# Kernel tuning notes

Hardware: AMD Instinct MI355X
Metric: run time of the kernel (lower is better)

Reference implementation:

```python
import jax, jax.numpy as jnp
import numpy as np

B, D, E, NF, FD, H = 8192, 1024, 6, 32, 32, 256
MINK, MAXK = 1, 4

def _lin(a, w, b):
    return a @ w.T + b

def setup_inputs():
    key = jax.random.key(0)
    it = iter(jax.random.split(key, 60))
    def nrm(shape, s=0.02):
        return jax.random.normal(next(it), shape, jnp.float32) * s
    z = lambda *s: jnp.zeros(s, jnp.float32)
    return dict(
        x=jax.random.normal(next(it), (B, D), jnp.float32),
        esp_patterns=nrm((E, D), 1.0),
        sim_w1=nrm((D // 2, D)), sim_b1=z(D // 2),
        sim_w2=nrm((E, D // 2)), sim_b2=z(E),
        rout_w1=nrm((D // 2, D + E)), rout_b1=z(D // 2),
        rout_w2=nrm((E, D // 2)), rout_b2=z(E),
        kpred_w1=nrm((16, 6)), kpred_b1=z(16),
        kpred_w2=nrm((1, 16)), kpred_b2=z(1),
        sp_v_w=nrm((D, D)), sp_v_b=z(D),
        sp_o_w=nrm((D, D)), sp_o_b=z(D),
        sp_q1_w=nrm((D, D)), sp_q1_b=z(D),
        sp_q2_w=nrm((D, D)), sp_q2_b=z(D),
        de_w1=nrm((H, D)), de_b1=z(H),
        de_w2=nrm((D, H)), de_b2=z(D),
        de_g_w=nrm((D, D)), de_g_b=z(D),
        cf_in_w=nrm((3 * FD, FD)), cf_in_b=z(3 * FD),
        cf_o_w=nrm((FD, FD)), cf_o_b=z(FD),
        cf_f_w=nrm((FD, FD)), cf_f_b=z(FD),
        hf_w1=nrm((H, D)), hf_b1=z(H),
        hf_w2=nrm((D, H)), hf_b2=z(D),
        tc_w=nrm((4, 1, 3), 0.2), tc_b=z(4),
        tf_w=nrm((1, 4), 0.2), tf_b=z(1),
        lt_w1=nrm((H, D)), lt_b1=z(H),
        lt_w2=nrm((D, H)), lt_b2=z(D),
        op_w=nrm((D, D)), op_b=z(D),
    )

def reference(x, esp_patterns, sim_w1, sim_b1, sim_w2, sim_b2, rout_w1, rout_b1, rout_w2, rout_b2,
              kpred_w1, kpred_b1, kpred_w2, kpred_b2, sp_v_w, sp_v_b, sp_o_w, sp_o_b,
              sp_q1_w, sp_q1_b, sp_q2_w, sp_q2_b, de_w1, de_b1, de_w2, de_b2, de_g_w, de_g_b,
              cf_in_w, cf_in_b, cf_o_w, cf_o_b, cf_f_w, cf_f_b, hf_w1, hf_b1, hf_w2, hf_b2,
              tc_w, tc_b, tf_w, tf_b, lt_w1, lt_b1, lt_w2, lt_b2, op_w, op_b):
    # ---- FeatureAnalyzer ----
    sparsity = (x == 0).astype(jnp.float32).mean(-1)
    var_u = jnp.var(x, axis=-1, ddof=1)            # torch default unbiased var
    magnitude = jnp.abs(x).max(-1)
    norm = jnp.linalg.norm(x, axis=-1)
    mean = x.mean(-1, keepdims=True)
    std = jnp.sqrt(var_u[:, None] + 1e-8)
    skew = (((x - mean) / std) ** 3).mean(-1)
    s_abs = -jnp.sort(-jnp.abs(x), axis=-1)        # descending
    top20 = int(0.2 * D)
    conc = s_abs[:, :top20].sum(-1) / (s_abs.sum(-1) + 1e-8)
    feats = jnp.stack([sparsity, var_u, magnitude, norm, skew, conc], -1)  # (B,6)
    # ---- IntelligentRouter ----
    spec = jax.nn.sigmoid(x @ esp_patterns.T + _lin(jax.nn.relu(_lin(x, sim_w1, sim_b1)), sim_w2, sim_b2))
    probs = jax.nn.softmax(_lin(jax.nn.relu(_lin(jnp.concatenate([x, spec], -1), rout_w1, rout_b1)), rout_w2, rout_b2), -1)
    k_ratio = jax.nn.sigmoid(_lin(jax.nn.relu(_lin(feats, kpred_w1, kpred_b1)), kpred_w2, kpred_b2))[:, 0]
    k_vals = MINK + (MAXK - MINK) * k_ratio
    k = jnp.clip(jnp.floor(jnp.median(k_vals)), MINK, MAXK).astype(jnp.int32)  # int(median) truncation
    tp, ti = jax.lax.top_k(probs, MAXK)
    gmask = jnp.arange(MAXK) < k
    gates = jax.nn.softmax(jnp.where(gmask, tp, -jnp.inf), -1)  # (B,MAXK)
    # ---- experts (eval mode: dropout = identity) ----
    # SparseQuadraticExpert: seq-len-1 MHA collapses to V->out projections
    att = _lin(_lin(x, sp_v_w, sp_v_b), sp_o_w, sp_o_b)
    e_sp = _lin(jax.nn.relu(_lin(att * x, sp_q1_w, sp_q1_b)), sp_q2_w, sp_q2_b)
    # DenseQuadraticExpert
    e_de = _lin(jax.nn.relu(_lin(x, de_w1, de_b1)), de_w2, de_b2) + jax.nn.sigmoid(_lin(x, de_g_w, de_g_b)) * x
    # CrossFieldQuadraticExpert: single-head attention over fields
    xf = x.reshape(-1, NF, FD)
    q, kk, v = jnp.split(_lin(xf, cf_in_w, cf_in_b), 3, axis=-1)
    attn = jax.nn.softmax(jnp.einsum('bqd,bkd->bqk', q, kk) / jnp.sqrt(jnp.float32(FD)), -1)
    att_f = _lin(jnp.einsum('bqk,bkd->bqd', attn, v), cf_o_w, cf_o_b)
    e_cf = _lin(att_f * xf, cf_f_w, cf_f_b).reshape(-1, D)
    # HighFreqQuadraticExpert
    filt = _lin(jnp.tanh(_lin(x, hf_w1, hf_b1)), hf_w2, hf_b2)
    e_hf = x + (filt - x) * x
    # TemporalQuadraticExpert (AdaptiveAvgPool1d(D) on length-D input == identity)
    conv = jax.nn.relu(jax.lax.conv_general_dilated(x[:, None, :], tc_w, (1,), [(1, 1)], dimension_numbers=('NCH', 'OIH', 'NCH')) + tc_b[None, :, None])
    wts = jax.nn.sigmoid(_lin(conv.transpose(0, 2, 1), tf_w, tf_b))[..., 0]  # (B,D)
    e_tp = (x * wts) * x
    # LongTailQuadraticExpert
    t = _lin(jax.nn.elu(_lin(x, lt_w1, lt_b1)), lt_w2, lt_b2)
    e_lt = jnp.sign(x) * jnp.sqrt(jnp.abs(t * x) + 1e-8)
    # ---- dispatch + combine ----
    stack = jnp.stack([e_sp, e_de, e_cf, e_hf, e_tp, e_lt], axis=1)  # (B,E,D)
    sel = jnp.take_along_axis(stack, ti[:, :, None], axis=1)         # (B,MAXK,D)
    comb = (gates[:, :, None] * sel).sum(1)
    return _lin(comb, op_w, op_b) + x  # output projection + residual; Identity norm (batch_norm=False)
```

## Files before the change

kernel.cpp:

```cpp
#include <hip/hip_runtime.h>
#include <stdint.h>

typedef unsigned short u16;
typedef __attribute__((ext_vector_type(2))) float f32x2;
typedef __attribute__((ext_vector_type(4))) float f32x4;
typedef __attribute__((ext_vector_type(4))) unsigned short u16x4;
typedef __attribute__((ext_vector_type(8))) short short8;

#define DEV static __device__ __forceinline__

DEV float bf2f(u16 u){ union{unsigned int i; float f;} v; v.i=((unsigned int)u)<<16; return v.f; }
DEV u16 f2bf(float f){ union{float f; unsigned int i;} v; v.f=f; unsigned int u=v.i;
  return (u16)((u + 0x7FFFu + ((u>>16)&1u))>>16); }
DEV float wred(float v){ for(int o=32;o;o>>=1) v += __shfl_xor(v,o); return v; }
DEV float wredmax(float v){ for(int o=32;o;o>>=1) v = fmaxf(v,__shfl_xor(v,o)); return v; }
DEV int wredi(int v){ for(int o=32;o;o>>=1) v += __shfl_xor(v,o); return v; }

DEV void gload16(const void* g, void* l){
  __builtin_amdgcn_global_load_lds((const __attribute__((address_space(1))) unsigned int*)g,
                                   (__attribute__((address_space(3))) unsigned int*)l, 16, 0, 0);
}

DEV float actf(int ACT, float v){
  if(ACT==1) return v>0.f?v:0.f;
  if(ACT==2) return 1.f/(1.f+__expf(-v));
  if(ACT==3) return tanhf(v);
  if(ACT==4) return v>0.f?v:(__expf(v)-1.f);
  return v;
}

__global__ void cvt_kernel(const float* __restrict__ s, u16* __restrict__ d, int n4){
  for(int i=blockIdx.x*blockDim.x+threadIdx.x; i<n4; i+=gridDim.x*blockDim.x){
    f32x4 v=((const f32x4*)s)[i];
    u16x4 o;
    #pragma unroll
    for(int j=0;j<4;++j) o[j]=f2bf(v[j]);
    ((u16x4*)d)[i]=o;
  }
}

__global__ void cvt6_kernel(
    const float* __restrict__ s0, const float* __restrict__ s1, const float* __restrict__ s2,
    const float* __restrict__ s3, const float* __restrict__ s4, const float* __restrict__ s5,
    u16* __restrict__ d0, u16* __restrict__ d1, u16* __restrict__ d2,
    u16* __restrict__ d3, u16* __restrict__ d4, u16* __restrict__ d5, int n4each){
  const float* ss[6]={s0,s1,s2,s3,s4,s5};
  u16* dd[6]={d0,d1,d2,d3,d4,d5};
  const int total=6*n4each;
  for(int i=blockIdx.x*blockDim.x+threadIdx.x; i<total; i+=gridDim.x*blockDim.x){
    int b=i/n4each, r=i-b*n4each;
    f32x4 v=((const f32x4*)ss[b])[r];
    u16x4 o;
    #pragma unroll
    for(int j=0;j<4;++j) o[j]=f2bf(v[j]);
    ((u16x4*)dd[b])[r]=o;
  }
}

__global__ void cvt_split(const float* __restrict__ s, u16* __restrict__ hi, u16* __restrict__ lo, int n4){
  for(int i=blockIdx.x*blockDim.x+threadIdx.x; i<n4; i+=gridDim.x*blockDim.x){
    f32x4 v=((const f32x4*)s)[i];
    u16x4 h,l;
    #pragma unroll
    for(int j=0;j<4;++j){ h[j]=f2bf(v[j]); l[j]=f2bf(v[j]-bf2f(h[j])); }
    ((u16x4*)hi)[i]=h; ((u16x4*)lo)[i]=l;
  }
}

__global__ void cvt_split_rw1(const float* __restrict__ src, u16* __restrict__ hi, u16* __restrict__ lo){
  for(int i=blockIdx.x*blockDim.x+threadIdx.x; i<512*1024; i+=gridDim.x*blockDim.x){
    int r=i>>10, c=i&1023;
    float v=src[(size_t)r*1030+c];
    u16 h=f2bf(v);
    hi[i]=h; lo[i]=f2bf(v-bf2f(h));
  }
}

__global__ __launch_bounds__(256) void transpose_bf(const float* __restrict__ src, u16* __restrict__ dst){
  __shared__ float t[32][33];
  const int bx=blockIdx.x&31, by=blockIdx.x>>5;
  const int lx=threadIdx.x&31, ly=threadIdx.x>>5;
  #pragma unroll
  for(int r=0;r<4;++r)
    t[ly+8*r][lx] = src[(size_t)(by*32+ly+8*r)*1024 + bx*32+lx];
  __syncthreads();
  #pragma unroll
  for(int r=0;r<4;++r)
    dst[(size_t)(bx*32+ly+8*r)*1024 + by*32+lx] = f2bf(t[lx][ly+8*r]);
}

__global__ __launch_bounds__(256) void bias_comp(const float* __restrict__ ow, const float* __restrict__ vb,
    const float* __restrict__ ob, float* __restrict__ bc){
  const int wv=threadIdx.x>>6, lane=threadIdx.x&63;
  const int rowi=blockIdx.x*4+wv;
  float s=0.f;
  const float* wr=ow+(size_t)rowi*1024;
  #pragma unroll
  for(int j=0;j<16;++j) s+=wr[j*64+lane]*vb[j*64+lane];
  s=wred(s);
  if(lane==0) bc[rowi]=ob[rowi]+s;
}

__global__ void pack_b768(const float* __restrict__ b0, const float* __restrict__ b1,
                          const float* __restrict__ b2, float* __restrict__ o){
  int i=blockIdx.x*blockDim.x+threadIdx.x;
  if(i<256) o[i]=b0[i];
  else if(i<512) o[i]=b1[i-256];
  else if(i<768) o[i]=b2[i-512];
}

__global__ void pack_b1024(const float* __restrict__ b0, const float* __restrict__ b1, float* __restrict__ o){
  int i=blockIdx.x*blockDim.x+threadIdx.x;
  if(i<512) o[i]=b0[i];
  else if(i<1024) o[i]=b1[i-512];
}

template<int ACT, int EPI>
__global__ __launch_bounds__(256) void gemm_bt(
    const u16* __restrict__ A, const u16* __restrict__ W,
    const float* __restrict__ bias, const u16* __restrict__ auxb,
    const float* __restrict__ auxf, const float* __restrict__ wsel,
    u16* __restrict__ comb, void* __restrict__ Cv, int M, int N, int K, int lda)
{
  __shared__ __align__(16) u16 lA[128*64];
  __shared__ __align__(16) u16 lB[128*64];
  const int tid=threadIdx.x, lane=tid&63, wv=tid>>6;
  const int wr=wv>>1, wc=wv&1;
  const int gx=gridDim.x;
  const int nwg=gx*gridDim.y;
  const int flat=blockIdx.y*gx+blockIdx.x;
  const int chunk=nwg>>3;
  const int nf=(flat&7)*chunk + (flat>>3);
  const int bn=(nf%gx)*128, bm=(nf/gx)*128;
  f32x4 acc[4][4];
  #pragma unroll
  for(int m=0;m<4;++m){
    #pragma unroll
    for(int n=0;n<4;++n) acc[m][n]=(f32x4)0.f;
  }
  const int srow = wv*8 + (lane>>3);
  const int scol = (lane&7)*8;
  for(int kt=0;kt<K;kt+=64){
    #pragma unroll
    for(int i=0;i<4;++i){
      gload16(A + (size_t)(bm + i*32 + srow)*lda + kt + scol, &lA[(i*32 + wv*8)*64]);
      gload16(W + (size_t)(bn + i*32 + srow)*K + kt + scol, &lB[(i*32 + wv*8)*64]);
    }
    __syncthreads();
    #pragma unroll
    for(int kk=0;kk<2;++kk){
      const int fr=lane&15, kc=kk*32+(lane>>4)*8;
      short8 af[4], bfr[4];
      #pragma unroll
      for(int m=0;m<4;++m) af[m]=*(const short8*)&lA[(wr*64+m*16+fr)*64+kc];
      #pragma unroll
      for(int n=0;n<4;++n) bfr[n]=*(const short8*)&lB[(wc*64+n*16+fr)*64+kc];
      #pragma unroll
      for(int m=0;m<4;++m){
        #pragma unroll
        for(int n=0;n<4;++n)
          acc[m][n]=__builtin_amdgcn_mfma_f32_16x16x32_bf16(af[m],bfr[n],acc[m][n],0,0,0);
      }
    }
    __syncthreads();
  }
  const int fr=lane&15, fq=lane>>4;
  #pragma unroll
  for(int m=0;m<4;++m){
    #pragma unroll
    for(int n=0;n<4;++n){
      const int col = bn + wc*64 + n*16 + fr;
      const float bv = bias ? bias[col] : 0.f;
      #pragma unroll
      for(int j=0;j<4;++j){
        const int row = bm + wr*64 + m*16 + fq*4 + j;
        const size_t idx = (size_t)row*N+col;
        float v = acc[m][n][j] + bv;
        if(ACT==5){
          v = (col<256) ? fmaxf(v,0.f) : (col<512 ? tanhf(v) : (v>0.f?v:(__expf(v)-1.f)));
        } else v = actf(ACT, v);
        if(EPI==0){ ((u16*)Cv)[idx]=f2bf(v); }
        else if(EPI==1){ ((float*)Cv)[idx]=v; }
        else if(EPI==2){ ((u16*)Cv)[idx]=f2bf(v*bf2f(auxb[idx])); }
        else if(EPI==3){ comb[idx]=f2bf(wsel[row*6+0]*v); }
        else if(EPI==4){ comb[idx]=f2bf(bf2f(comb[idx])+wsel[row*6+1]*(v + bf2f(auxb[idx])*auxf[idx])); }
        else if(EPI==5){ float x0=bf2f(auxb[idx]); comb[idx]=f2bf(bf2f(comb[idx])+wsel[row*6+3]*(x0+(v-x0)*x0)); }
        else if(EPI==6){
          float x0=bf2f(auxb[idx]);
          float sg=(x0>0.f)?1.f:((x0<0.f)?-1.f:0.f);
          comb[idx]=f2bf(bf2f(comb[idx])+wsel[row*6+5]*sg*sqrtf(fabsf(v*x0)+1e-8f));
        }
        else { ((float*)Cv)[idx]=v+auxf[idx]; }
      }
    }
  }
}

__global__ __launch_bounds__(256) void gemm_split2(
    const u16* __restrict__ Ah, const u16* __restrict__ Al,
    const u16* __restrict__ Wh, const u16* __restrict__ Wl,
    const float* __restrict__ bias, float* __restrict__ C, int M, int N, int K)
{
  const int LDL=40;
  __shared__ __align__(16) u16 lAh[128*40], lAl[128*40], lBh[128*40], lBl[128*40];
  const int tid=threadIdx.x, lane=tid&63, wv=tid>>6;
  const int wr=wv>>1, wc=wv&1;
  const int nwg=gridDim.x;
  const int wg=(blockIdx.x%8)*(nwg/8)+blockIdx.x/8;
  const int bx=wg&7, by=wg>>3;
  const int bn=bx*128, bm=by*128;
  f32x4 acc[4][4];
  #pragma unroll
  for(int m=0;m<4;++m){
    #pragma unroll
    for(int n=0;n<4;++n) acc[m][n]=(f32x4)0.f;
  }
  const int srow=tid>>2, scol=(tid&3)*8;
  for(int kt=0;kt<K;kt+=32){
    short8 rah[2],ral[2],rbh[2],rbl[2];
    #pragma unroll
    for(int i=0;i<2;++i){
      size_t ao=(size_t)(bm+i*64+srow)*K+kt+scol;
      size_t bo=(size_t)(bn+i*64+srow)*K+kt+scol;
      rah[i]=*(const short8*)(Ah+ao); ral[i]=*(const short8*)(Al+ao);
      rbh[i]=*(const short8*)(Wh+bo); rbl[i]=*(const short8*)(Wl+bo);
    }
    __syncthreads();
    #pragma unroll
    for(int i=0;i<2;++i){
      int d=(i*64+srow)*LDL+scol;
      *(short8*)&lAh[d]=rah[i]; *(short8*)&lAl[d]=ral[i];
      *(short8*)&lBh[d]=rbh[i]; *(short8*)&lBl[d]=rbl[i];
    }
    __syncthreads();
    const int fr=lane&15, kc=(lane>>4)*8;
    short8 ah[4],al[4],bh[4],bl[4];
    #pragma unroll
    for(int m=0;m<4;++m){ int r=(wr*64+m*16+fr)*LDL+kc; ah[m]=*(const short8*)&lAh[r]; al[m]=*(const short8*)&lAl[r]; }
    #pragma unroll
    for(int n=0;n<4;++n){ int r=(wc*64+n*16+fr)*LDL+kc; bh[n]=*(const short8*)&lBh[r]; bl[n]=*(const short8*)&lBl[r]; }
    #pragma unroll
    for(int m=0;m<4;++m){
      #pragma unroll
      for(int n=0;n<4;++n){
        acc[m][n]=__builtin_amdgcn_mfma_f32_16x16x32_bf16(ah[m],bh[n],acc[m][n],0,0,0);
        acc[m][n]=__builtin_amdgcn_mfma_f32_16x16x32_bf16(ah[m],bl[n],acc[m][n],0,0,0);
        acc[m][n]=__builtin_amdgcn_mfma_f32_16x16x32_bf16(al[m],bh[n],acc[m][n],0,0,0);
      }
    }
  }
  const int fr=lane&15, fq=lane>>4;
  #pragma unroll
  for(int m=0;m<4;++m){
    #pragma unroll
    for(int n=0;n<4;++n){
      const int col = bn + wc*64 + n*16 + fr;
      const float bv = bias[col];
      #pragma unroll
      for(int j=0;j<4;++j){
        const int row = bm + wr*64 + m*16 + fq*4 + j;
        float v = acc[m][n][j] + bv;
        if(col<512) v=fmaxf(v,0.f);
        C[(size_t)row*N+col] = v;
      }
    }
  }
}

__global__ __launch_bounds__(256) void feats_kernel(const float* __restrict__ x,
    const float* __restrict__ kw1, const float* __restrict__ kb1,
    const float* __restrict__ kw2, const float* __restrict__ kb2,
    float* __restrict__ kvals)
{
  const int lane=threadIdx.x&63, wv=threadIdx.x>>6;
  const int row=blockIdx.x*4+wv;
  const float* xr=x+(size_t)row*1024;
  float xv[16]; unsigned int cd[16];
  float s=0.f, ss=0.f, sa=0.f, nz=0.f, amax=0.f;
  #pragma unroll
  for(int t=0;t<4;++t){
    f32x4 v=((const f32x4*)xr)[t*64+lane];
    #pragma unroll
    for(int j=0;j<4;++j){
      float f=v[j];
      union{float f;unsigned int i;} c; c.f=f;
      xv[t*4+j]=f; cd[t*4+j]=c.i&0x7fffffffu;
      s+=f; ss+=f*f; float a=fabsf(f); sa+=a; amax=fmaxf(amax,a); if(f==0.f) nz+=1.f;
    }
  }
  s=wred(s); ss=wred(ss); sa=wred(sa); nz=wred(nz); amax=wredmax(amax);
  const float mean=s/1024.f;
  const float var=(ss - s*mean)/1023.f;
  const float inv=1.f/sqrtf(var+1e-8f);
  float sk=0.f;
  #pragma unroll
  for(int j=0;j<16;++j){ float z=(xv[j]-mean)*inv; sk+=z*z*z; }
  sk=wred(sk);
  unsigned int lo=0u, hi=0x7f800000u;
  while(hi-lo>1u){
    unsigned int mid=(lo+hi)>>1;
    int c=0;
    #pragma unroll
    for(int j=0;j<16;++j) c += (cd[j] >= mid);
    c=wredi(c);
    if(c>=204) lo=mid; else hi=mid;
  }
  const unsigned int T=lo;
  float sg=0.f, cg=0.f;
  #pragma unroll
  for(int j=0;j<16;++j){ if(cd[j] > T){ sg+=fabsf(xv[j]); cg+=1.f; } }
  sg=wred(sg); cg=wred(cg);
  if(lane==0){
    union{unsigned int i;float f;} tv; tv.i=T;
    float conc=(sg + (204.f-cg)*tv.f)/(sa + 1e-8f);
    float feats[6]={ nz/1024.f, var, amax, sqrtf(ss), sk/1024.f, conc };
    float out=kb2[0];
    #pragma unroll
    for(int i=0;i<16;++i){
      float hv=kb1[i];
      #pragma unroll
      for(int j=0;j<6;++j) hv+=kw1[i*6+j]*feats[j];
      hv=fmaxf(hv,0.f);
      out+=kw2[i]*hv;
    }
    kvals[row]=1.f + 3.f*(1.f/(1.f+__expf(-out)));
  }
}

__global__ __launch_bounds__(256) void median_kernel(const float* __restrict__ kvals, int* __restrict__ kint){
  __shared__ unsigned int v[8192];
  __shared__ int hist4[4*257];
  __shared__ unsigned int selT;
  __shared__ int selR;
  const int tid=threadIdx.x, lane=tid&63, wv=tid>>6;
  for(int i=tid;i<8192;i+=256){ union{float f;unsigned int u;} c; c.f=kvals[i]; v[i]=c.u; }
  __syncthreads();
  unsigned int res[2];
  for(int t=0;t<2;++t){
    int r = 8192 - (4096+t) + 1;
    unsigned int prefix=0u;
    for(int lvl=0;lvl<4;++lvl){
      const int shift=24-lvl*8;
      const unsigned int pmask = (lvl==0)?0u:(0xFFFFFFFFu<<(shift+8));
      for(int i=tid;i<4*257;i+=256) hist4[i]=0;
      __syncthreads();
      for(int i=tid;i<8192;i+=256){
        unsigned int c=v[i];
        if((c&pmask)==prefix) atomicAdd(&hist4[wv*257+((c>>shift)&0xFFu)],1);
      }
      __syncthreads();
      if(wv==0){
        int h[4]; int ls=0;
        #pragma unroll
        for(int b=0;b<4;++b){
          int bin=lane*4+b;
          h[b]=hist4[bin]+hist4[257+bin]+hist4[514+bin]+hist4[771+bin];
          ls+=h[b];
        }
        int pfx=ls;
        #pragma unroll
        for(int off=1;off<64;off<<=1){ int tt=__shfl_up(pfx,off); if(lane>=off) pfx+=tt; }
        int total=__shfl(pfx,63);
        int cgt = total - pfx;
        #pragma unroll
        for(int b=3;b>=0;--b){
          if(cgt < r && r <= cgt + h[b]){
            selT = prefix | ((unsigned int)(lane*4+b)<<shift);
            selR = r - cgt;
          }
          cgt += h[b];
        }
      }
      __syncthreads();
      prefix=selT; r=selR;
      __syncthreads();
    }
    res[t]=prefix;
  }
  if(tid==0){
    union{unsigned int u; float f;} a,b; a.u=res[0]; b.u=res[1];
    float med=0.5f*(a.f+b.f);
    int k=(int)floorf(med);
    k = k<1?1:(k>4?4:k);
    *kint=k;
  }
}

__global__ __launch_bounds__(256) void spec_kernel(const float* __restrict__ x, const float* __restrict__ h,
    const float* __restrict__ esp, const float* __restrict__ w2, const float* __restrict__ b2,
    float* __restrict__ spec){
  const int wv=threadIdx.x>>6, lane=threadIdx.x&63;
  const int row=blockIdx.x*4+wv;
  const float* xr=x+(size_t)row*1024;
  const float* hr=h+(size_t)row*1024;
  float xv[16], hv[8];
  #pragma unroll
  for(int j=0;j<16;++j) xv[j]=xr[j*64+lane];
  #pragma unroll
  for(int j=0;j<8;++j) hv[j]=hr[j*64+lane];
  for(int e=0;e<6;++e){
    float s=0.f;
    #pragma unroll
    for(int j=0;j<16;++j) s+=xv[j]*esp[e*1024+j*64+lane];
    #pragma unroll
    for(int j=0;j<8;++j) s+=hv[j]*w2[e*512+j*64+lane];
    s=wred(s);
    if(lane==0) spec[row*6+e]=1.f/(1.f+__expf(-(s+b2[e])));
  }
}

__global__ void rout_fix(float* __restrict__ h, const float* __restrict__ spec, const float* __restrict__ rw1){
  const int total=8192*128;
  for(int i=blockIdx.x*blockDim.x+threadIdx.x;i<total;i+=gridDim.x*blockDim.x){
    int row=i>>7, j0=(i&127)*4;
    const float* sp=&spec[row*6];
    f32x4 hv=*(f32x4*)&h[(size_t)row*1024+512+j0];
    #pragma unroll
    for(int j=0;j<4;++j){
      float v=hv[j];
      int col=j0+j;
      #pragma unroll
      for(int e=0;e<6;++e) v+=sp[e]*rw1[(size_t)col*1030+1024+e];
      hv[j]=fmaxf(v,0.f);
    }
    *(f32x4*)&h[(size_t)row*1024+512+j0]=hv;
  }
}

__global__ __launch_bounds__(256) void probs_kernel(const float* __restrict__ h, const float* __restrict__ w2,
    const float* __restrict__ b2, float* __restrict__ probs){
  const int wv=threadIdx.x>>6, lane=threadIdx.x&63;
  const int row=blockIdx.x*4+wv;
  const float* hr=h+(size_t)row*1024+512;
  float hv[8];
  #pragma unroll
  for(int j=0;j<8;++j) hv[j]=hr[j*64+lane];
  float lg[6];
  #pragma unroll
  for(int e=0;e<6;++e){
    float s=0.f;
    #pragma unroll
    for(int j=0;j<8;++j) s+=hv[j]*w2[e*512+j*64+lane];
    lg[e]=wred(s)+b2[e];
  }
  if(lane==0){
    float m=lg[0];
    #pragma unroll
    for(int e=1;e<6;++e) m=fmaxf(m,lg[e]);
    float den=0.f, ex[6];
    #pragma unroll
    for(int e=0;e<6;++e){ ex[e]=__expf(lg[e]-m); den+=ex[e]; }
    #pragma unroll
    for(int e=0;e<6;++e) probs[row*6+e]=ex[e]/den;
  }
}

__global__ void gates_kernel(const float* __restrict__ probs, const int* __restrict__ kint,
                             float* __restrict__ wsel){
  const int r=blockIdx.x*blockDim.x+threadIdx.x;
  if(r>=8192) return;
  const int k=*kint;
  float p[6];
  #pragma unroll
  for(int e=0;e<6;++e) p[e]=probs[r*6+e];
  float w[6]={0,0,0,0,0,0};
  bool used[6]={false,false,false,false,false,false};
  int idx[4]; float val[4];
  #pragma unroll
  for(int j=0;j<4;++j){
    int bi=0; float bv=-1e30f;
    #pragma unroll
    for(int e=0;e<6;++e) if(!used[e] && p[e]>bv){ bv=p[e]; bi=e; }
    used[bi]=true; idx[j]=bi; val[j]=bv;
  }
  float m=val[0], den=0.f, g[4]={0,0,0,0};
  for(int j=0;j<k;++j){ g[j]=__expf(val[j]-m); den+=g[j]; }
  for(int j=0;j<k;++j) w[idx[j]]=g[j]/den;
  #pragma unroll
  for(int e=0;e<6;++e) wsel[r*6+e]=w[e];
}

__global__ __launch_bounds__(256) void cf_kernel(const float* __restrict__ x,
    const float* __restrict__ w_in, const float* __restrict__ b_in,
    const float* __restrict__ w_o, const float* __restrict__ b_o,
    const float* __restrict__ w_f, const float* __restrict__ b_f,
    const float* __restrict__ wsel, u16* __restrict__ comb){
  __shared__ __align__(16) u16 smem[6400 + 4*6144];
  const int tid=threadIdx.x, wv=tid>>6, lane=tid&63;
  const int fr=lane&15, fq=lane>>4;
  for(int i=tid;i<5120;i+=256){
    float v=(i<3072)? w_in[i] : (i<4096? w_o[i-3072] : w_f[i-4096]);
    smem[(i>>5)*40 + (i&31)] = f2bf(v);
  }
  u16* wb   = smem + 6400 + wv*6144;
  float* xfl= (float*)wb;
  u16* bufA = wb + 2304;
  u16* bufB = bufA + 1280;
  u16* bufC = bufB + 1280;
  const int row = blockIdx.x*4 + wv;
  const float* xr = x + (size_t)row*1024;
  #pragma unroll
  for(int t=0;t<4;++t){
    f32x4 v = ((const f32x4*)xr)[t*64+lane];
    int e=(t*64+lane)*4;
    *(f32x4*)&xfl[(e>>5)*36 + (e&31)] = v;
  }
  __syncthreads();
  short8 xa[2];
  #pragma unroll
  for(int ft=0;ft<2;++ft){
    f32x4 a=*(const f32x4*)&xfl[(ft*16+fr)*36 + fq*8];
    f32x4 b=*(const f32x4*)&xfl[(ft*16+fr)*36 + fq*8 + 4];
    short8 s;
    s[0]=(short)f2bf(a[0]); s[1]=(short)f2bf(a[1]); s[2]=(short)f2bf(a[2]); s[3]=(short)f2bf(a[3]);
    s[4]=(short)f2bf(b[0]); s[5]=(short)f2bf(b[1]); s[6]=(short)f2bf(b[2]); s[7]=(short)f2bf(b[3]);
    xa[ft]=s;
  }
  f32x4 acc1[2][6];
  #pragma unroll
  for(int ct=0;ct<6;++ct){
    short8 wfrag=*(const short8*)&smem[(ct*16+fr)*40 + fq*8];
    #pragma unroll
    for(int ft=0;ft<2;++ft)
      acc1[ft][ct]=__builtin_amdgcn_mfma_f32_16x16x32_bf16(xa[ft],wfrag,(f32x4)0.f,0,0,0);
  }
  float bi[6];
  #pragma unroll
  for(int ct=0;ct<6;++ct) bi[ct]=b_in[ct*16+fr];
  #pragma unroll
  for(int ct=0;ct<6;++ct){
    #pragma unroll
    for(int ft=0;ft<2;++ft){
      #pragma unroll
      for(int j=0;j<4;++j){
        u16 h=f2bf(acc1[ft][ct][j]+bi[ct]);
        int rg=ft*16+fq*4+j, cg=ct*16+fr;
        if(cg<32)      bufA[rg*40+cg]=h;
        else if(cg<64) bufB[rg*40+(cg-32)]=h;
        else           bufC[(cg-64)*40+rg]=h;
      }
    }
  }
  __syncthreads();
  short8 qa0=*(const short8*)&bufA[fr*40+fq*8];
  short8 qa1=*(const short8*)&bufA[(16+fr)*40+fq*8];
  short8 kb0=*(const short8*)&bufB[fr*40+fq*8];
  short8 kb1=*(const short8*)&bufB[(16+fr)*40+fq*8];
  f32x4 aS[2][2];
  aS[0][0]=__builtin_amdgcn_mfma_f32_16x16x32_bf16(qa0,kb0,(f32x4)0.f,0,0,0);
  aS[0][1]=__builtin_amdgcn_mfma_f32_16x16x32_bf16(qa0,kb1,(f32x4)0.f,0,0,0);
  aS[1][0]=__builtin_amdgcn_mfma_f32_16x16x32_bf16(qa1,kb0,(f32x4)0.f,0,0,0);
  aS[1][1]=__builtin_amdgcn_mfma_f32_16x16x32_bf16(qa1,kb1,(f32x4)0.f,0,0,0);
  const float scale=0.17677669529663687f;
  #pragma unroll
  for(int rt=0;rt<2;++rt){
    #pragma unroll
    for(int j=0;j<4;++j){
      float e0=aS[rt][0][j]*scale, e1=aS[rt][1][j]*scale;
      float m=fmaxf(e0,e1);
      #pragma unroll
      for(int o=1;o<16;o<<=1) m=fmaxf(m,__shfl_xor(m,o));
      e0=__expf(e0-m); e1=__expf(e1-m);
      float den=e0+e1;
      #pragma unroll
      for(int o=1;o<16;o<<=1) den+=__shfl_xor(den,o);
      float inv=1.f/den;
      bufA[(rt*16+fq*4+j)*40 + fr]      = f2bf(e0*inv);
      bufA[(rt*16+fq*4+j)*40 + 16+fr]   = f2bf(e1*inv);
    }
  }
  __syncthreads();
  short8 pa0=*(const short8*)&bufA[fr*40+fq*8];
  short8 pa1=*(const short8*)&bufA[(16+fr)*40+fq*8];
  short8 vb0=*(const short8*)&bufC[fr*40+fq*8];
  short8 vb1=*(const short8*)&bufC[(16+fr)*40+fq*8];
  f32x4 aA[2][2];
  aA[0][0]=__builtin_amdgcn_mfma_f32_16x16x32_bf16(pa0,vb0,(f32x4)0.f,0,0,0);
  aA[0][1]=__builtin_amdgcn_mfma_f32_16x16x32_bf16(pa0,vb1,(f32x4)0.f,0,0,0);
  aA[1][0]=__builtin_amdgcn_mfma_f32_16x16x32_bf16(pa1,vb0,(f32x4)0.f,0,0,0);
  aA[1][1]=__builtin_amdgcn_mfma_f32_16x16x32_bf16(pa1,vb1,(f32x4)0.f,0,0,0);
  #pragma unroll
  for(int rt=0;rt<2;++rt)
    #pragma unroll
    for(int dt=0;dt<2;++dt)
      #pragma unroll
      for(int j=0;j<4;++j)
        bufB[(rt*16+fq*4+j)*40 + dt*16+fr]=f2bf(aA[rt][dt][j]);
  __syncthreads();
  short8 aa0=*(const short8*)&bufB[fr*40+fq*8];
  short8 aa1=*(const short8*)&bufB[(16+fr)*40+fq*8];
  short8 ob0=*(const short8*)&smem[(96+fr)*40+fq*8];
  short8 ob1=*(const short8*)&smem[(112+fr)*40+fq*8];
  f32x4 aF[2][2];
  aF[0][0]=__builtin_amdgcn_mfma_f32_16x16x32_bf16(aa0,ob0,(f32x4)0.f,0,0,0);
  aF[0][1]=__builtin_amdgcn_mfma_f32_16x16x32_bf16(aa0,ob1,(f32x4)0.f,0,0,0);
  aF[1][0]=__builtin_amdgcn_mfma_f32_16x16x32_bf16(aa1,ob0,(f32x4)0.f,0,0,0);
  aF[1][1]=__builtin_amdgcn_mfma_f32_16x16x32_bf16(aa1,ob1,(f32x4)0.f,0,0,0);
  float bo[2]={b_o[fr], b_o[16+fr]};
  #pragma unroll
  for(int rt=0;rt<2;++rt){
    #pragma unroll
    for(int dt=0;dt<2;++dt){
      #pragma unroll
      for(int j=0;j<4;++j){
        int fld=rt*16+fq*4+j, d=dt*16+fr;
        float attf=aF[rt][dt][j]+bo[dt];
        bufC[fld*40+d]=f2bf(attf*xfl[fld*36+d]);
      }
    }
  }
  __syncthreads();
  short8 pr0=*(const short8*)&bufC[fr*40+fq*8];
  short8 pr1=*(const short8*)&bufC[(16+fr)*40+fq*8];
  short8 fb0=*(const short8*)&smem[(128+fr)*40+fq*8];
  short8 fb1=*(const short8*)&smem[(144+fr)*40+fq*8];
  f32x4 aE[2][2];
  aE[0][0]=__builtin_amdgcn_mfma_f32_16x16x32_bf16(pr0,fb0,(f32x4)0.f,0,0,0);
  aE[0][1]=__builtin_amdgcn_mfma_f32_16x16x32_bf16(pr0,fb1,(f32x4)0.f,0,0,0);
  aE[1][0]=__builtin_amdgcn_mfma_f32_16x16x32_bf16(pr1,fb0,(f32x4)0.f,0,0,0);
  aE[1][1]=__builtin_amdgcn_mfma_f32_16x16x32_bf16(pr1,fb1,(f32x4)0.f,0,0,0);
  float bff[2]={b_f[fr], b_f[16+fr]};
  const float w2=wsel[row*6+2];
  u16* cb=&comb[(size_t)row*1024];
  #pragma unroll
  for(int rt=0;rt<2;++rt){
    #pragma unroll
    for(int dt=0;dt<2;++dt){
      #pragma unroll
      for(int j=0;j<4;++j){
        int fld=rt*16+fq*4+j, d=dt*16+fr;
        u16 old=cb[fld*32+d];
        cb[fld*32+d]=f2bf(bf2f(old)+w2*(aE[rt][dt][j]+bff[dt]));
      }
    }
  }
}

__global__ __launch_bounds__(256) void tp_kernel(const float* __restrict__ x,
    const float* __restrict__ wsel, const u16* __restrict__ comb,
    const float* __restrict__ tcw, const float* __restrict__ tcb,
    const float* __restrict__ tfw, const float* __restrict__ tfb,
    u16* __restrict__ obf){
  __shared__ float xs[1026];
  const int row=blockIdx.x, tid=threadIdx.x;
  f32x4 u=((const f32x4*)(x+(size_t)row*1024))[tid];
  #pragma unroll
  for(int j=0;j<4;++j) xs[1+4*tid+j]=u[j];
  if(tid==0){ xs[0]=0.f; xs[1025]=0.f; }
  __syncthreads();
  const float w4=wsel[row*6+4];
  float tc[4][3], tb[4], tf[4];
  #pragma unroll
  for(int o=0;o<4;++o){
    #pragma unroll
    for(int kh=0;kh<3;++kh) tc[o][kh]=tcw[o*3+kh];
    tb[o]=tcb[o]; tf[o]=tfw[o];
  }
  const float tfb0=tfb[0];
  u16x4 cv=((const u16x4*)(comb+(size_t)row*1024))[tid];
  u16x4 ov;
  #pragma unroll
  for(int j=0;j<4;++j){
    const int d=4*tid+j;
    float pre=tfb0;
    #pragma unroll
    for(int o=0;o<4;++o){
      float c=tb[o]+tc[o][0]*xs[d]+tc[o][1]*xs[d+1]+tc[o][2]*xs[d+2];
      pre+=tf[o]*fmaxf(c,0.f);
    }
    float wt=1.f/(1.f+__expf(-pre));
    float xv=xs[1+d];
    ov[j]=f2bf(bf2f(cv[j])+w4*xv*xv*wt);
  }
  ((u16x4*)(obf+(size_t)row*1024))[tid]=ov;
}

extern "C" void kernel_launch(void* const* d_in, const int* in_sizes, int n_in,
                              void* d_out, int out_size, void* d_ws, size_t ws_size,
                              hipStream_t stream)
{
  const float* x     =(const float*)d_in[0];
  const float* esp   =(const float*)d_in[1];
  const float* sim_w1=(const float*)d_in[2],  *sim_b1=(const float*)d_in[3];
  const float* sim_w2=(const float*)d_in[4],  *sim_b2=(const float*)d_in[5];
  const float* rout_w1=(const float*)d_in[6], *rout_b1=(const float*)d_in[7];
  const float* rout_w2=(const float*)d_in[8], *rout_b2=(const float*)d_in[9];
  const float* kw1=(const float*)d_in[10], *kb1=(const float*)d_in[11];
  const float* kw2=(const float*)d_in[12], *kb2=(const float*)d_in[13];
  const float* spv_w=(const float*)d_in[14], *spv_b=(const float*)d_in[15];
  const float* spo_w=(const float*)d_in[16], *spo_b=(const float*)d_in[17];
  const float* spq1_w=(const float*)d_in[18], *spq1_b=(const float*)d_in[19];
  const float* spq2_w=(const float*)d_in[20], *spq2_b=(const float*)d_in[21];
  const float* de_w1=(const float*)d_in[22], *de_b1=(const float*)d_in[23];
  const float* de_w2=(const float*)d_in[24], *de_b2=(const float*)d_in[25];
  const float* de_gw=(const float*)d_in[26], *de_gb=(const float*)d_in[27];
  const float* cf_inw=(const float*)d_in[28], *cf_inb=(const float*)d_in[29];
  const float* cf_ow=(const float*)d_in[30], *cf_ob=(const float*)d_in[31];
  const float* cf_fw=(const float*)d_in[32], *cf_fb=(const float*)d_in[33];
  const float* hf_w1=(const float*)d_in[34], *hf_b1=(const float*)d_in[35];
  const float* hf_w2=(const float*)d_in[36], *hf_b2=(const float*)d_in[37];
  const float* tc_w=(const float*)d_in[38], *tc_b=(const float*)d_in[39];
  const float* tf_w=(const float*)d_in[40], *tf_b=(const float*)d_in[41];
  const float* lt_w1=(const float*)d_in[42], *lt_b1=(const float*)d_in[43];
  const float* lt_w2=(const float*)d_in[44], *lt_b2=(const float*)d_in[45];
  const float* op_w=(const float*)d_in[46], *op_b=(const float*)d_in[47];
  float* out=(float*)d_out;
  (void)in_sizes; (void)n_in; (void)out_size; (void)ws_size;

  constexpr int NB=8192;
  const size_t BD=(size_t)NB*1024;
  char* base=(char*)d_ws; size_t off=0;
  auto carve=[&](size_t n)->void*{ void* q=base+off; off+=(n+255)&~(size_t)255; return q; };
  u16*  comb =(u16*)carve(BD*2);
  u16*  bufA =(u16*)carve(BD*2);
  u16*  bufB =(u16*)carve(BD*2);
  u16*  x_hi =(u16*)carve(BD*2);
  u16*  x_lo =(u16*)carve(BD*2);
  float* h1024=(float*)carve(BD*4);
  u16*  h768 =(u16*)carve((size_t)NB*768*2);
  u16* w1024h=(u16*)carve((size_t)1024*1024*2);
  u16* w1024l=(u16*)carve((size_t)1024*1024*2);
  u16* spv_bf =(u16*)carve((size_t)1024*1024*2);
  u16* spo_bf =(u16*)carve((size_t)1024*1024*2);
  u16* spq1_bf=(u16*)carve((size_t)1024*1024*2);
  u16* spq2_bf=(u16*)carve((size_t)1024*1024*2);
  u16* w768_bf=(u16*)carve((size_t)768*1024*2);
  u16* dew2_bf=(u16*)carve((size_t)1024*256*2);
  u16* degw_bf=(u16*)carve((size_t)1024*1024*2);
  u16* hfw2_bf=(u16*)carve((size_t)1024*256*2);
  u16* ltw2_bf=(u16*)carve((size_t)1024*256*2);
  u16* opw_bf =(u16*)carve((size_t)1024*1024*2);
  u16* spvT_bf=(u16*)carve((size_t)1024*1024*2);
  float* bc   =(float*)carve((size_t)1024*4);
  float* b768 =(float*)carve((size_t)768*4);
  float* b1024=(float*)carve((size_t)1024*4);
  float* spec=(float*)carve((size_t)NB*6*4);
  float* probs=(float*)carve((size_t)NB*6*4);
  float* wsel=(float*)carve((size_t)NB*6*4);
  float* kvals=(float*)carve((size_t)NB*4);
  int*   kint=(int*)carve(256);

  const dim3 blk(256);
  const dim3 gEW(2048);
  auto cgrid=[&](int n4)->dim3{ int g=(n4+255)/256; return dim3(g>2048?2048:g); };

  cvt_split<<<cgrid(2097152),blk,0,stream>>>(x, x_hi, x_lo, 2097152);
  cvt_split<<<cgrid(131072),blk,0,stream>>>(sim_w1, w1024h, w1024l, 131072);
  cvt_split_rw1<<<cgrid(131072),blk,0,stream>>>(rout_w1, w1024h+524288, w1024l+524288);
  cvt6_kernel<<<cgrid(6*262144),blk,0,stream>>>(spv_w,spo_w,spq1_w,spq2_w,de_gw,op_w,
                                                spv_bf,spo_bf,spq1_bf,spq2_bf,degw_bf,opw_bf, 262144);
  cvt6_kernel<<<cgrid(6*65536),blk,0,stream>>>(de_w1,de_w2,hf_w1,hf_w2,lt_w1,lt_w2,
                                               w768_bf,dew2_bf,w768_bf+262144,hfw2_bf,w768_bf+524288,ltw2_bf, 65536);
  transpose_bf<<<dim3(1024),blk,0,stream>>>(spv_w, spvT_bf);
  bias_comp<<<dim3(256),blk,0,stream>>>(spo_w, spv_b, spo_b, bc);
  pack_b768<<<dim3(3),blk,0,stream>>>(de_b1, hf_b1, lt_b1, b768);
  pack_b1024<<<dim3(4),blk,0,stream>>>(sim_b1, rout_b1, b1024);

  feats_kernel<<<dim3(2048),blk,0,stream>>>(x, kw1,kb1,kw2,kb2, kvals);
  median_kernel<<<dim3(1),blk,0,stream>>>(kvals, kint);
  gemm_split2<<<dim3(512),blk,0,stream>>>(x_hi,x_lo, w1024h,w1024l, b1024, h1024, NB,1024,1024);
  spec_kernel<<<gEW,blk,0,stream>>>(x, h1024, esp, sim_w2, sim_b2, spec);
  rout_fix<<<gEW,blk,0,stream>>>(h1024, spec, rout_w1);
  probs_kernel<<<gEW,blk,0,stream>>>(h1024, rout_w2, rout_b2, probs);
  gates_kernel<<<dim3(32),blk,0,stream>>>(probs, kint, wsel);

  gemm_bt<0,1><<<dim3(8,8),blk,0,stream>>>(spo_bf, spvT_bf, nullptr, nullptr, nullptr, nullptr, nullptr, h1024, 1024,1024,1024,1024);
  cvt_kernel<<<cgrid(262144),blk,0,stream>>>(h1024, spv_bf, 262144);

  gemm_bt<0,2><<<dim3(8,64),blk,0,stream>>>(x_hi, spv_bf, bc, x_hi, nullptr, nullptr, nullptr, bufB, NB,1024,1024,1024);
  gemm_bt<1,0><<<dim3(8,64),blk,0,stream>>>(bufB, spq1_bf, spq1_b, nullptr, nullptr, nullptr, nullptr, bufA, NB,1024,1024,1024);
  gemm_bt<0,3><<<dim3(8,64),blk,0,stream>>>(bufA, spq2_bf, spq2_b, nullptr, nullptr, wsel, comb, nullptr, NB,1024,1024,1024);

  gemm_bt<5,0><<<dim3(6,64),blk,0,stream>>>(x_hi, w768_bf, b768, nullptr, nullptr, nullptr, nullptr, h768, NB,768,1024,1024);

  gemm_bt<2,0><<<dim3(8,64),blk,0,stream>>>(x_hi, degw_bf, de_gb, nullptr, nullptr, nullptr, nullptr, bufB, NB,1024,1024,1024);
  gemm_bt<0,4><<<dim3(8,64),blk,0,stream>>>(h768, dew2_bf, de_b2, bufB, x, wsel, comb, nullptr, NB,1024,256,768);

  cf_kernel<<<dim3(2048),blk,0,stream>>>(x, cf_inw, cf_inb, cf_ow, cf_ob, cf_fw, cf_fb, wsel, comb);

  gemm_bt<0,5><<<dim3(8,64),blk,0,stream>>>(h768+256, hfw2_bf, hf_b2, x_hi, nullptr, wsel, comb, nullptr, NB,1024,256,768);

  gemm_bt<0,6><<<dim3(8,64),blk,0,stream>>>(h768+512, ltw2_bf, lt_b2, x_hi, nullptr, wsel, comb, nullptr, NB,1024,256,768);

  tp_kernel<<<dim3(NB),blk,0,stream>>>(x, wsel, comb, tc_w, tc_b, tf_w, tf_b, bufB);

  gemm_bt<0,7><<<dim3(8,64),blk,0,stream>>>(bufB, opw_bf, op_b, nullptr, x, nullptr, nullptr, out, NB,1024,1024,1024);
}
```

Baseline: 580.0 us.

## Fuse router stages into one kernel and fold x bf16 split into feats

Result: faster. 564.0 us (-2.8%).

```diff
diff --git a/kernel.cpp b/kernel.cpp
--- a/kernel.cpp
+++ b/kernel.cpp
@@ -270,23 +270,28 @@
 __global__ __launch_bounds__(256) void feats_kernel(const float* __restrict__ x,
     const float* __restrict__ kw1, const float* __restrict__ kb1,
     const float* __restrict__ kw2, const float* __restrict__ kb2,
-    float* __restrict__ kvals)
+    float* __restrict__ kvals, u16* __restrict__ x_hi, u16* __restrict__ x_lo)
 {
   const int lane=threadIdx.x&63, wv=threadIdx.x>>6;
   const int row=blockIdx.x*4+wv;
   const float* xr=x+(size_t)row*1024;
+  u16x4* hio=(u16x4*)(x_hi+(size_t)row*1024);
+  u16x4* loo=(u16x4*)(x_lo+(size_t)row*1024);
   float xv[16]; unsigned int cd[16];
   float s=0.f, ss=0.f, sa=0.f, nz=0.f, amax=0.f;
   #pragma unroll
   for(int t=0;t<4;++t){
     f32x4 v=((const f32x4*)xr)[t*64+lane];
+    u16x4 h,l;
     #pragma unroll
     for(int j=0;j<4;++j){
       float f=v[j];
       union{float f;unsigned int i;} c; c.f=f;
       xv[t*4+j]=f; cd[t*4+j]=c.i&0x7fffffffu;
+      h[j]=f2bf(f); l[j]=f2bf(f-bf2f(h[j]));
       s+=f; ss+=f*f; float a=fabsf(f); sa+=a; amax=fmaxf(amax,a); if(f==0.f) nz+=1.f;
     }
+    hio[t*64+lane]=h; loo[t*64+lane]=l;
   }
   s=wred(s); ss=wred(ss); sa=wred(sa); nz=wred(nz); amax=wredmax(amax);
   const float mean=s/1024.f;
@@ -386,98 +391,75 @@
   }
 }
 
-__global__ __launch_bounds__(256) void spec_kernel(const float* __restrict__ x, const float* __restrict__ h,
-    const float* __restrict__ esp, const float* __restrict__ w2, const float* __restrict__ b2,
-    float* __restrict__ spec){
+__global__ __launch_bounds__(256) void router_kernel(const float* __restrict__ x,
+    const float* __restrict__ h, const float* __restrict__ esp,
+    const float* __restrict__ w2s, const float* __restrict__ b2s,
+    const float* __restrict__ rw1, const float* __restrict__ w2r,
+    const float* __restrict__ b2r, const int* __restrict__ kint,
+    float* __restrict__ wsel)
+{
   const int wv=threadIdx.x>>6, lane=threadIdx.x&63;
   const int row=blockIdx.x*4+wv;
   const float* xr=x+(size_t)row*1024;
   const float* hr=h+(size_t)row*1024;
-  float xv[16], hv[8];
+  float xv[16], h0[8], h1[8];
   #pragma unroll
   for(int j=0;j<16;++j) xv[j]=xr[j*64+lane];
   #pragma unroll
-  for(int j=0;j<8;++j) hv[j]=hr[j*64+lane];
+  for(int j=0;j<8;++j){ h0[j]=hr[j*64+lane]; h1[j]=hr[512+j*64+lane]; }
+  float spec[6];
+  #pragma unroll
   for(int e=0;e<6;++e){
     float s=0.f;
     #pragma unroll
     for(int j=0;j<16;++j) s+=xv[j]*esp[e*1024+j*64+lane];
     #pragma unroll
-    for(int j=0;j<8;++j) s+=hv[j]*w2[e*512+j*64+lane];
+    for(int j=0;j<8;++j) s+=h0[j]*w2s[e*512+j*64+lane];
     s=wred(s);
-    if(lane==0) spec[row*6+e]=1.f/(1.f+__expf(-(s+b2[e])));
-  }
-}
-
-__global__ void rout_fix(float* __restrict__ h, const float* __restrict__ spec, const float* __restrict__ rw1){
-  const int total=8192*128;
-  for(int i=blockIdx.x*blockDim.x+threadIdx.x;i<total;i+=gridDim.x*blockDim.x){
-    int row=i>>7, j0=(i&127)*4;
-    const float* sp=&spec[row*6];
-    f32x4 hv=*(f32x4*)&h[(size_t)row*1024+512+j0];
-    #pragma unroll
-    for(int j=0;j<4;++j){
-      float v=hv[j];
-      int col=j0+j;
-      #pragma unroll
-      for(int e=0;e<6;++e) v+=sp[e]*rw1[(size_t)col*1030+1024+e];
-      hv[j]=fmaxf(v,0.f);
-    }
-    *(f32x4*)&h[(size_t)row*1024+512+j0]=hv;
-  }
-}
-
-__global__ __launch_bounds__(256) void probs_kernel(const float* __restrict__ h, const float* __restrict__ w2,
-    const float* __restrict__ b2, float* __restrict__ probs){
-  const int wv=threadIdx.x>>6, lane=threadIdx.x&63;
-  const int row=blockIdx.x*4+wv;
-  const float* hr=h+(size_t)row*1024+512;
-  float hv[8];
-  #pragma unroll
-  for(int j=0;j<8;++j) hv[j]=hr[j*64+lane];
-  float lg[6];
+    spec[e]=1.f/(1.f+__expf(-(s+b2s[e])));
+  }
+  #pragma unroll
+  for(int j=0;j<8;++j){
+    int col=j*64+lane;
+    float v=h1[j];
+    #pragma unroll
+    for(int e=0;e<6;++e) v+=spec[e]*rw1[(size_t)col*1030+1024+e];
+    h1[j]=fmaxf(v,0.f);
+  }
+  float p[6];
+  float m=-1e30f;
   #pragma unroll
   for(int e=0;e<6;++e){
     float s=0.f;
     #pragma unroll
-    for(int j=0;j<8;++j) s+=hv[j]*w2[e*512+j*64+lane];
-    lg[e]=wred(s)+b2[e];
-  }
+    for(int j=0;j<8;++j) s+=h1[j]*w2r[e*512+j*64+lane];
+    p[e]=wred(s)+b2r[e];
+    m=fmaxf(m,p[e]);
+  }
+  float den=0.f;
+  #pragma unroll
+  for(int e=0;e<6;++e){ p[e]=__expf(p[e]-m); den+=p[e]; }
+  float invd=1.f/den;
+  #pragma unroll
+  for(int e=0;e<6;++e) p[e]*=invd;
   if(lane==0){
-    float m=lg[0];
-    #pragma unroll
-    for(int e=1;e<6;++e) m=fmaxf(m,lg[e]);
-    float den=0.f, ex[6];
-    #pragma unroll
-    for(int e=0;e<6;++e){ ex[e]=__expf(lg[e]-m); den+=ex[e]; }
-    #pragma unroll
-    for(int e=0;e<6;++e) probs[row*6+e]=ex[e]/den;
-  }
-}
-
-__global__ void gates_kernel(const float* __restrict__ probs, const int* __restrict__ kint,
-                             float* __restrict__ wsel){
-  const int r=blockIdx.x*blockDim.x+threadIdx.x;
-  if(r>=8192) return;
-  const int k=*kint;
-  float p[6];
-  #pragma unroll
-  for(int e=0;e<6;++e) p[e]=probs[r*6+e];
-  float w[6]={0,0,0,0,0,0};
-  bool used[6]={false,false,false,false,false,false};
-  int idx[4]; float val[4];
-  #pragma unroll
-  for(int j=0;j<4;++j){
-    int bi=0; float bv=-1e30f;
-    #pragma unroll
-    for(int e=0;e<6;++e) if(!used[e] && p[e]>bv){ bv=p[e]; bi=e; }
-    used[bi]=true; idx[j]=bi; val[j]=bv;
-  }
-  float m=val[0], den=0.f, g[4]={0,0,0,0};
-  for(int j=0;j<k;++j){ g[j]=__expf(val[j]-m); den+=g[j]; }
-  for(int j=0;j<k;++j) w[idx[j]]=g[j]/den;
-  #pragma unroll
-  for(int e=0;e<6;++e) wsel[r*6+e]=w[e];
+    const int k=*kint;
+    float w[6]={0,0,0,0,0,0};
+    bool used[6]={false,false,false,false,false,false};
+    int idx[4]; float val[4];
+    #pragma unroll
+    for(int j=0;j<4;++j){
+      int bi=0; float bv=-1e30f;
+      #pragma unroll
+      for(int e=0;e<6;++e) if(!used[e] && p[e]>bv){ bv=p[e]; bi=e; }
+      used[bi]=true; idx[j]=bi; val[j]=bv;
+    }
+    float mm=val[0], dd=0.f, g[4]={0,0,0,0};
+    for(int j=0;j<k;++j){ g[j]=__expf(val[j]-mm); dd+=g[j]; }
+    for(int j=0;j<k;++j) w[idx[j]]=g[j]/dd;
+    float* o=&wsel[(size_t)row*6];
+    o[0]=w[0]; o[1]=w[1]; o[2]=w[2]; o[3]=w[3]; o[4]=w[4]; o[5]=w[5];
+  }
 }
 
 __global__ __launch_bounds__(256) void cf_kernel(const float* __restrict__ x,
@@ -734,17 +716,16 @@
   float* bc   =(float*)carve((size_t)1024*4);
   float* b768 =(float*)carve((size_t)768*4);
   float* b1024=(float*)carve((size_t)1024*4);
-  float* spec=(float*)carve((size_t)NB*6*4);
-  float* probs=(float*)carve((size_t)NB*6*4);
   float* wsel=(float*)carve((size_t)NB*6*4);
   float* kvals=(float*)carve((size_t)NB*4);
   int*   kint=(int*)carve(256);
 
   const dim3 blk(256);
-  const dim3 gEW(2048);
   auto cgrid=[&](int n4)->dim3{ int g=(n4+255)/256; return dim3(g>2048?2048:g); };
 
-  cvt_split<<<cgrid(2097152),blk,0,stream>>>(x, x_hi, x_lo, 2097152);
+  feats_kernel<<<dim3(2048),blk,0,stream>>>(x, kw1,kb1,kw2,kb2, kvals, x_hi, x_lo);
+  median_kernel<<<dim3(1),blk,0,stream>>>(kvals, kint);
+
   cvt_split<<<cgrid(131072),blk,0,stream>>>(sim_w1, w1024h, w1024l, 131072);
   cvt_split_rw1<<<cgrid(131072),blk,0,stream>>>(rout_w1, w1024h+524288, w1024l+524288);
   cvt6_kernel<<<cgrid(6*262144),blk,0,stream>>>(spv_w,spo_w,spq1_w,spq2_w,de_gw,op_w,
@@ -756,13 +737,8 @@
   pack_b768<<<dim3(3),blk,0,stream>>>(de_b1, hf_b1, lt_b1, b768);
   pack_b1024<<<dim3(4),blk,0,stream>>>(sim_b1, rout_b1, b1024);
 
-  feats_kernel<<<dim3(2048),blk,0,stream>>>(x, kw1,kb1,kw2,kb2, kvals);
-  median_kernel<<<dim3(1),blk,0,stream>>>(kvals, kint);
   gemm_split2<<<dim3(512),blk,0,stream>>>(x_hi,x_lo, w1024h,w1024l, b1024, h1024, NB,1024,1024);
-  spec_kernel<<<gEW,blk,0,stream>>>(x, h1024, esp, sim_w2, sim_b2, spec);
-  rout_fix<<<gEW,blk,0,stream>>>(h1024, spec, rout_w1);
-  probs_kernel<<<gEW,blk,0,stream>>>(h1024, rout_w2, rout_b2, probs);
-  gates_kernel<<<dim3(32),blk,0,stream>>>(probs, kint, wsel);
+  router_kernel<<<dim3(2048),blk,0,stream>>>(x, h1024, esp, sim_w2, sim_b2, rout_w1, rout_w2, rout_b2, kint, wsel);
 
   gemm_bt<0,1><<<dim3(8,8),blk,0,stream>>>(spo_bf, spvT_bf, nullptr, nullptr, nullptr, nullptr, nullptr, h1024, 1024,1024,1024,1024);
   cvt_kernel<<<cgrid(262144),blk,0,stream>>>(h1024, spv_bf, 262144);
```
